# Performance work log

Measured on AMD Instinct MI355X. Metric: run time of the kernel, lower is better.

## Reference

```python
import jax, jax.numpy as jnp
import numpy as np

B = 8
WS = 7; NH = 8; HD = 16; C = 128; HP = 56; SHIFT = 3; L = HP * HP
SCALE = HD ** -0.5


def _rel_pos_index():
    coords = np.stack(np.meshgrid(np.arange(WS), np.arange(WS), indexing='ij')).reshape(2, -1)
    rel = (coords[:, :, None] - coords[:, None, :]).transpose(1, 2, 0)
    rel[:, :, 0] += WS - 1
    rel[:, :, 1] += WS - 1
    rel[:, :, 0] *= 2 * WS - 1
    return rel.sum(-1)  # (49, 49) int


def _attn_mask():
    img = np.zeros((HP, HP))
    cnt = 0
    for h in (slice(0, -WS), slice(-WS, -SHIFT), slice(-SHIFT, None)):
        for w in (slice(0, -WS), slice(-WS, -SHIFT), slice(-SHIFT, None)):
            img[h, w] = cnt
            cnt += 1
    m = img.reshape(HP // WS, WS, HP // WS, WS).transpose(0, 2, 1, 3).reshape(-1, WS * WS)
    am = m[:, None, :] - m[:, :, None]
    return np.where(am != 0, -100.0, 0.0).astype(np.float32)  # (64, 49, 49)


REL_IDX = _rel_pos_index()
ATTN_MASK = jnp.asarray(_attn_mask())


def _ln(x, g, b):
    mu = x.mean(-1, keepdims=True)
    v = ((x - mu) ** 2).mean(-1, keepdims=True)
    return (x - mu) / jnp.sqrt(v + 1e-5) * g + b


def setup_inputs() -> dict:
    key = jax.random.key(0)
    ks = iter(jax.random.split(key, 40))
    n = lambda shape: jax.random.normal(next(ks), shape, dtype=jnp.float32) * 0.02
    z = lambda shape: jnp.zeros(shape, dtype=jnp.float32)
    o = lambda shape: jnp.ones(shape, dtype=jnp.float32)
    return dict(
        infrared=jax.random.normal(next(ks), (B, 1, 224, 224), dtype=jnp.float32),
        visible=jax.random.normal(next(ks), (B, 1, 224, 224), dtype=jnp.float32),
        patch_w=n((16, C)), patch_b=z((C,)),
        pn_g=o((C,)), pn_b=z((C,)),
        pos_embed=n((1, L, C)),
        norm1_g=o((2, C)), norm1_b=z((2, C)),
        qkv_w=n((2, C, 3 * C)), qkv_b=z((2, 3 * C)),
        proj_w=n((2, C, C)), proj_b=z((2, C)),
        norm2_g=o((2, C)), norm2_b=z((2, C)),
        fc1_w=n((2, C, 4 * C)), fc1_b=z((2, 4 * C)),
        fc2_w=n((2, 4 * C, C)), fc2_b=z((2, C)),
        rpb=n((2, (2 * WS - 1) ** 2, NH)),
        normf_g=o((C,)), normf_b=z((C,)),
        head1_w=n((C, 256)), head1_b=z((256,)),
        head2_w=n((256, 1)), head2_b=z((1,)),
    )


def reference(infrared, visible, patch_w, patch_b, pn_g, pn_b, pos_embed,
              norm1_g, norm1_b, qkv_w, qkv_b, proj_w, proj_b,
              norm2_g, norm2_b, fc1_w, fc1_b, fc2_w, fc2_b, rpb,
              normf_g, normf_b, head1_w, head1_b, head2_w, head2_b):
    Bv = visible.shape[0]
    # 4x4 stride-4 conv on 1-channel input == patchify + matmul
    x = visible.reshape(Bv, HP, 4, HP, 4).transpose(0, 1, 3, 2, 4).reshape(Bv, L, 16)
    x = _ln(x @ patch_w + patch_b, pn_g, pn_b) + pos_embed  # (B, 3136, 128)

    def win_attn(xw, i, mask):
        Bn, N = xw.shape[0], WS * WS
        qkv = (xw @ qkv_w[i] + qkv_b[i]).reshape(Bn, N, 3, NH, HD).transpose(2, 0, 3, 1, 4)
        q, k, v = qkv[0], qkv[1], qkv[2]
        attn = jnp.einsum('bhnd,bhmd->bhnm', q * SCALE, k)  # (Bn, H, 49, 49)
        bias = rpb[i][REL_IDX.reshape(-1)].reshape(N, N, NH).transpose(2, 0, 1)
        attn = attn + bias[None]
        if mask is not None:
            attn = attn.reshape(Bv, -1, NH, N, N) + mask[None, :, None]
            attn = attn.reshape(Bn, NH, N, N)
        attn = jax.nn.softmax(attn, axis=-1)
        out = jnp.einsum('bhnm,bhmd->bhnd', attn, v).transpose(0, 2, 1, 3).reshape(Bn, N, C)
        return out @ proj_w[i] + proj_b[i]

    def block(x, i, shift):
        shortcut = x
        h = _ln(x, norm1_g[i], norm1_b[i]).reshape(Bv, HP, HP, C)
        if shift:
            h = jnp.roll(h, (-SHIFT, -SHIFT), (1, 2))
        w = h.reshape(Bv, 8, WS, 8, WS, C).transpose(0, 1, 3, 2, 4, 5).reshape(-1, WS * WS, C)
        w = win_attn(w, i, ATTN_MASK if shift else None)
        h = w.reshape(Bv, 8, 8, WS, WS, C).transpose(0, 1, 3, 2, 4, 5).reshape(Bv, HP, HP, C)
        if shift:
            h = jnp.roll(h, (SHIFT, SHIFT), (1, 2))
        x = shortcut + h.reshape(Bv, L, C)  # drop_path is identity at inference
        m = _ln(x, norm2_g[i], norm2_b[i])
        m = jax.nn.gelu(m @ fc1_w[i] + fc1_b[i]) @ fc2_w[i] + fc2_b[i]
        return x + m

    x = block(x, 0, False)
    x = block(x, 1, True)
    x = jax.nn.relu(_ln(x, normf_g, normf_b))          # (B, 3136, 128)
    x = x.reshape(Bv, C, HP, HP)                       # raw view, as in torch code
    x = jnp.repeat(jnp.repeat(x, 4, axis=2), 4, axis=3)  # nearest 56 -> 224
    x = x.reshape(Bv, 224 * 224, C)                    # raw view
    x = jax.nn.relu(x @ head1_w + head1_b) @ head2_w + head2_b
    return x.reshape(Bv, 1, 224, 224)
```

## Files before the change

### kernel.cpp

```cpp
#include <hip/hip_runtime.h>
#include <math.h>

#define DEV __device__ __forceinline__

constexpr int B_   = 8;
constexpr int NTOK = 25088;
constexpr int WGc  = 512;
constexpr int N2c  = 49;
constexpr int HDc  = 16;
constexpr int NHc  = 8;
constexpr float SCALEq = 0.25f;

typedef _Float16 f16x8 __attribute__((ext_vector_type(8)));
typedef float    f32x4 __attribute__((ext_vector_type(4)));

DEV float wave_sum(float v) {
#pragma unroll
  for (int m = 32; m >= 1; m >>= 1) v += __shfl_xor(v, m);
  return v;
}

DEV float gelu_f(float x) {
  float y = 0.7978845608028654f * (x + 0.044715f * x * x * x);
  return x / (1.f + __expf(-2.f * y));
}

DEV int win_map(int row, int shift) {
  int wg = row / 49, n = row - wg * 49;
  int b = wg >> 6, win = wg & 63;
  int sh = ((win >> 3) * 7) + n / 7;
  int sw = ((win & 7) * 7) + (n % 7);
  sh += shift; if (sh >= 56) sh -= 56;
  sw += shift; if (sw >= 56) sw -= 56;
  return b * 3136 + sh * 56 + sw;
}

DEV void split8(const float* __restrict__ x, ushort* hp, ushort* lp) {
  f16x8 h, l;
#pragma unroll
  for (int j = 0; j < 8; ++j) {
    float v = x[j];
    _Float16 hh = (_Float16)v;
    h[j] = hh;
    l[j] = (_Float16)(v - (float)hh);
  }
  *(f16x8*)hp = h;
  *(f16x8*)lp = l;
}

__global__ __launch_bounds__(128)
void patch_k(const float* __restrict__ vis, const float* __restrict__ pw,
             const float* __restrict__ pb, const float* __restrict__ g,
             const float* __restrict__ bb, const float* __restrict__ pos,
             float* __restrict__ X) {
  int row = blockIdx.x;
  int c = threadIdx.x;
  int b = row / 3136, l = row - b * 3136;
  int hp = l / 56, wp = l - hp * 56;
  __shared__ float p[16];
  __shared__ float red[2];
  if (c < 16) {
    int r = c >> 2, cc = c & 3;
    p[c] = vis[(long)b * 50176 + (hp * 4 + r) * 224 + wp * 4 + cc];
  }
  __syncthreads();
  float t = pb[c];
#pragma unroll
  for (int k = 0; k < 16; ++k) t = fmaf(p[k], pw[k * 128 + c], t);
  float s = wave_sum(t);
  if ((c & 63) == 0) red[c >> 6] = s;
  __syncthreads();
  float mu = (red[0] + red[1]) * (1.f / 128.f);
  __syncthreads();
  float d = t - mu;
  float s2 = wave_sum(d * d);
  if ((c & 63) == 0) red[c >> 6] = s2;
  __syncthreads();
  float var = (red[0] + red[1]) * (1.f / 128.f);
  float o = d * rsqrtf(var + 1e-5f) * g[c] + bb[c] + pos[(long)l * 128 + c];
  X[(long)row * 128 + c] = o;
}

__global__ __launch_bounds__(256)
void ln_k(const float* __restrict__ Xi, float* __restrict__ Out,
          const float* __restrict__ g, const float* __restrict__ b, int do_relu) {
  int row = blockIdx.x * 4 + (threadIdx.x >> 6);
  int lane = threadIdx.x & 63;
  long base = (long)row * 128 + lane * 2;
  float2 v = *(const float2*)&Xi[base];
  float mu = wave_sum(v.x + v.y) * (1.f / 128.f);
  float dx = v.x - mu, dy = v.y - mu;
  float var = wave_sum(dx * dx + dy * dy) * (1.f / 128.f);
  float r = rsqrtf(var + 1e-5f);
  float2 gg = *(const float2*)&g[lane * 2];
  float2 bb = *(const float2*)&b[lane * 2];
  float ox = dx * r * gg.x + bb.x;
  float oy = dy * r * gg.y + bb.y;
  if (do_relu) { ox = fmaxf(ox, 0.f); oy = fmaxf(oy, 0.f); }
  *(float2*)&Out[base] = make_float2(ox, oy);
}

template<int OUT_MODE, int ACT, int GATHER_A>
__global__ __launch_bounds__(256)
void mgemm_k(const float* __restrict__ A, const float* __restrict__ W,
             const float* __restrict__ bias, float* __restrict__ Out,
             int N, int K, int lda, int shift) {
  __shared__ __align__(16) ushort Ah[2048], Al[2048];
  __shared__ __align__(16) ushort Bh[4096], Bl[4096];
  int tid = threadIdx.x;
  int m0 = blockIdx.x * 64, n0 = blockIdx.y * 128;
  int lane = tid & 63, wid = tid >> 6;
  int wm = wid >> 1, wn = wid & 1;

  f32x4 acc[2][4];
#pragma unroll
  for (int mi = 0; mi < 2; ++mi)
#pragma unroll
    for (int ni = 0; ni < 4; ++ni) acc[mi][ni] = (f32x4){0.f, 0.f, 0.f, 0.f};

  int sr = tid >> 2;
  int sk8 = tid & 3;
  long asrc = GATHER_A ? (long)win_map(m0 + sr, shift) * lda
                       : (long)(m0 + sr) * lda;
  int achunk = ((sr >> 4) * 64 + sk8 * 16 + (sr & 15)) * 8;

  int bn0_ = tid & 127, bk80 = tid >> 7;
  int bn1_ = bn0_, bk81 = bk80 + 2;
  int bchunk0 = ((bn0_ >> 4) * 64 + bk80 * 16 + (bn0_ & 15)) * 8;
  int bchunk1 = ((bn1_ >> 4) * 64 + bk81 * 16 + (bn1_ & 15)) * 8;

  float areg[8], breg0[8], breg1[8];
  auto loadA = [&](int k0) {
    float4 t0 = *(const float4*)&A[asrc + k0 + sk8 * 8];
    float4 t1 = *(const float4*)&A[asrc + k0 + sk8 * 8 + 4];
    areg[0] = t0.x; areg[1] = t0.y; areg[2] = t0.z; areg[3] = t0.w;
    areg[4] = t1.x; areg[5] = t1.y; areg[6] = t1.z; areg[7] = t1.w;
  };
  auto loadB = [&](int k0) {
#pragma unroll
    for (int j = 0; j < 8; ++j)
      breg0[j] = W[(long)(k0 + bk80 * 8 + j) * N + n0 + bn0_];
#pragma unroll
    for (int j = 0; j < 8; ++j)
      breg1[j] = W[(long)(k0 + bk81 * 8 + j) * N + n0 + bn1_];
  };

  loadA(0); loadB(0);
  for (int k0 = 0; k0 < K; k0 += 32) {
    __syncthreads();
    split8(areg, &Ah[achunk], &Al[achunk]);
    split8(breg0, &Bh[bchunk0], &Bl[bchunk0]);
    split8(breg1, &Bh[bchunk1], &Bl[bchunk1]);
    __syncthreads();
    if (k0 + 32 < K) { loadA(k0 + 32); loadB(k0 + 32); }

    f16x8 ah[2], al[2], bh[4], bl[4];
#pragma unroll
    for (int mi = 0; mi < 2; ++mi) {
      int c = ((wm * 2 + mi) * 64 + lane) * 8;
      ah[mi] = *(const f16x8*)&Ah[c];
      al[mi] = *(const f16x8*)&Al[c];
    }
#pragma unroll
    for (int ni = 0; ni < 4; ++ni) {
      int c = ((wn * 4 + ni) * 64 + lane) * 8;
      bh[ni] = *(const f16x8*)&Bh[c];
      bl[ni] = *(const f16x8*)&Bl[c];
    }
#pragma unroll
    for (int mi = 0; mi < 2; ++mi)
#pragma unroll
      for (int ni = 0; ni < 4; ++ni) {
        acc[mi][ni] = __builtin_amdgcn_mfma_f32_16x16x32_f16(ah[mi], bh[ni], acc[mi][ni], 0, 0, 0);
        acc[mi][ni] = __builtin_amdgcn_mfma_f32_16x16x32_f16(ah[mi], bl[ni], acc[mi][ni], 0, 0, 0);
        acc[mi][ni] = __builtin_amdgcn_mfma_f32_16x16x32_f16(al[mi], bh[ni], acc[mi][ni], 0, 0, 0);
      }
  }

  int r4 = (lane >> 4) * 4, cb = lane & 15;
#pragma unroll
  for (int mi = 0; mi < 2; ++mi) {
#pragma unroll
    for (int rr = 0; rr < 4; ++rr) {
      int row = m0 + wm * 32 + mi * 16 + r4 + rr;
      int dst = (OUT_MODE == 2) ? win_map(row, shift) : row;
#pragma unroll
      for (int ni = 0; ni < 4; ++ni) {
        int col = n0 + wn * 64 + ni * 16 + cb;
        float val = acc[mi][ni][rr] + bias[col];
        if (ACT == 1) val = gelu_f(val);
        if (OUT_MODE == 0) {
          Out[(long)row * N + col] = val;
        } else if (OUT_MODE == 1) {
          int t = col >> 7, cc = col & 127, h = cc >> 4, d = cc & 15;
          if (t == 0) val *= SCALEq;
          int wg = row / 49, n = row - wg * 49;
          Out[((((long)t * WGc + wg) * NHc + h) * N2c + n) * HDc + d] = val;
        } else {
          Out[(long)dst * 128 + col] += val;
        }
      }
    }
  }
}

__global__ __launch_bounds__(256)
void attn_k(const float* __restrict__ QKV, float* __restrict__ AO,
            const float* __restrict__ rpb, int shift) {
  int wg = blockIdx.x >> 3;
  int h  = blockIdx.x & 7;
  int tid = threadIdx.x;
  __shared__ float Qs[49][17], Ks[49][17], Vs[49][17];
  __shared__ float S[49][50];
  const float* Qp = QKV + (((long)0 * WGc + wg) * NHc + h) * N2c * HDc;
  const float* Kp = QKV + (((long)1 * WGc + wg) * NHc + h) * N2c * HDc;
  const float* Vp = QKV + (((long)2 * WGc + wg) * NHc + h) * N2c * HDc;
  for (int idx = tid; idx < 49 * 16; idx += 256) {
    int n = idx >> 4, d = idx & 15;
    Qs[n][d] = Qp[idx]; Ks[n][d] = Kp[idx]; Vs[n][d] = Vp[idx];
  }
  __syncthreads();
  int win = wg & 63, wy = win >> 3, wx = win & 7;
  for (int idx = tid; idx < 49 * 49; idx += 256) {
    int i = idx / 49, j = idx - i * 49;
    float s = 0.f;
#pragma unroll
    for (int d = 0; d < 16; ++d) s = fmaf(Qs[i][d], Ks[j][d], s);
    int pyi = i / 7, pxi = i - pyi * 7, pyj = j / 7, pxj = j - pyj * 7;
    int rel = (pyi - pyj + 6) * 13 + (pxi - pxj + 6);
    s += rpb[rel * 8 + h];
    if (shift) {
      int shi = wy * 7 + pyi, swi = wx * 7 + pxi;
      int shj = wy * 7 + pyj, swj = wx * 7 + pxj;
      int ri = (shi < 49 ? 0 : (shi < 53 ? 1 : 2)) * 3 + (swi < 49 ? 0 : (swi < 53 ? 1 : 2));
      int rj = (shj < 49 ? 0 : (shj < 53 ? 1 : 2)) * 3 + (swj < 49 ? 0 : (swj < 53 ? 1 : 2));
      if (ri != rj) s -= 100.f;
    }
    S[i][j] = s;
  }
  __syncthreads();
  int lane = tid & 63, wv = tid >> 6;
  for (int i = wv; i < 49; i += 4) {
    float v = lane < 49 ? S[i][lane] : -1e30f;
    float m = v;
#pragma unroll
    for (int d = 32; d >= 1; d >>= 1) m = fmaxf(m, __shfl_xor(m, d));
    float e = lane < 49 ? __expf(v - m) : 0.f;
    float s = e;
#pragma unroll
    for (int d = 32; d >= 1; d >>= 1) s += __shfl_xor(s, d);
    if (lane < 49) S[i][lane] = e / s;
  }
  __syncthreads();
  for (int idx = tid; idx < 49 * 16; idx += 256) {
    int i = idx >> 4, d = idx & 15;
    float o = 0.f;
    for (int j = 0; j < 49; ++j) o = fmaf(S[i][j], Vs[j][d], o);
    AO[((long)wg * 49 + i) * 128 + h * 16 + d] = o;
  }
}

__global__ __launch_bounds__(256)
void w1sum_k(const float* __restrict__ W1, float* __restrict__ W1s) {
  int a = blockIdx.x, c = threadIdx.x;
  float s = W1[(4 * a + 0) * 256 + c] + W1[(4 * a + 1) * 256 + c] +
            W1[(4 * a + 2) * 256 + c] + W1[(4 * a + 3) * 256 + c];
  W1s[a * 256 + c] = s;
}

__global__ __launch_bounds__(512)
void head_k(const float* __restrict__ Y, const float* __restrict__ W1s,
            const float* __restrict__ b1, const float* __restrict__ W2,
            const float* __restrict__ b2, float* __restrict__ Out) {
  __shared__ float As[32][128];
  __shared__ float Ws[32][256];
  int tid = threadIdx.x;
  int m0 = blockIdx.x * 128;

  {
    int arow = tid >> 2;
    int rg = m0 + arow;
    int b = rg / 50176;
    int r = rg - b * 50176;
    int ch = r / 392;
    int s = r - ch * 392;
    long ybase = (long)b * 401408 + (long)ch * 3136;
    int a0 = (tid & 3) * 8;
    int tb = s * 128 + a0 * 4;
#pragma unroll
    for (int e = 0; e < 8; ++e) {
      int t = tb + e * 4;
      int H = t / 224, Wp = t - H * 224;
      As[a0 + e][arow] = Y[ybase + (H >> 2) * 56 + (Wp >> 2)];
    }
  }
  for (int i = tid; i < 2048; i += 512) {
    int id4 = i * 4;
    *(float4*)&Ws[id4 >> 8][id4 & 255] = *(const float4*)&W1s[id4];
  }
  __syncthreads();

  int tx = tid & 31, ty = tid >> 5;
  float acc[8][8] = {};
#pragma unroll 4
  for (int k = 0; k < 32; ++k) {
    float4 a0 = *(const float4*)&As[k][ty * 8];
    float4 a1 = *(const float4*)&As[k][ty * 8 + 4];
    float a8[8] = {a0.x, a0.y, a0.z, a0.w, a1.x, a1.y, a1.z, a1.w};
    float w8[8];
#pragma unroll
    for (int cc = 0; cc < 8; ++cc) w8[cc] = Ws[k][tx + 32 * cc];
#pragma unroll
    for (int rr = 0; rr < 8; ++rr)
#pragma unroll
      for (int cc = 0; cc < 8; ++cc)
        acc[rr][cc] = fmaf(a8[rr], w8[cc], acc[rr][cc]);
  }

  float b2v = b2[0];
#pragma unroll
  for (int rr = 0; rr < 8; ++rr) {
    float p = 0.f;
#pragma unroll
    for (int cc = 0; cc < 8; ++cc) {
      int col = tx + 32 * cc;
      float hval = fmaxf(acc[rr][cc] + b1[col], 0.f);
      p = fmaf(hval, W2[col], p);
    }
#pragma unroll
    for (int d = 16; d >= 1; d >>= 1) p += __shfl_xor(p, d);
    if (tx == 0) Out[(long)m0 + ty * 8 + rr] = p + b2v;
  }
}

extern "C" void kernel_launch(void* const* d_in, const int* in_sizes, int n_in,
                              void* d_out, int out_size, void* d_ws, size_t ws_size,
                              hipStream_t stream) {
  const float* visible = (const float*)d_in[1];
  const float* patch_w = (const float*)d_in[2];
  const float* patch_b = (const float*)d_in[3];
  const float* pn_g    = (const float*)d_in[4];
  const float* pn_b    = (const float*)d_in[5];
  const float* pos     = (const float*)d_in[6];
  const float* norm1_g = (const float*)d_in[7];
  const float* norm1_b = (const float*)d_in[8];
  const float* qkv_w   = (const float*)d_in[9];
  const float* qkv_b   = (const float*)d_in[10];
  const float* proj_w  = (const float*)d_in[11];
  const float* proj_b  = (const float*)d_in[12];
  const float* norm2_g = (const float*)d_in[13];
  const float* norm2_b = (const float*)d_in[14];
  const float* fc1_w   = (const float*)d_in[15];
  const float* fc1_b   = (const float*)d_in[16];
  const float* fc2_w   = (const float*)d_in[17];
  const float* fc2_b   = (const float*)d_in[18];
  const float* rpb     = (const float*)d_in[19];
  const float* normf_g = (const float*)d_in[20];
  const float* normf_b = (const float*)d_in[21];
  const float* h1w     = (const float*)d_in[22];
  const float* h1b     = (const float*)d_in[23];
  const float* h2w     = (const float*)d_in[24];
  const float* h2b     = (const float*)d_in[25];
  float* out = (float*)d_out;

  float* X   = (float*)d_ws;
  float* XN  = X  + (long)NTOK * 128;
  float* BIG = XN + (long)NTOK * 128;
  float* QKV = BIG;
  float* AO  = BIG + (long)NTOK * 384;
  float* Hb  = BIG;
  float* Y   = XN;
  float* W1s = BIG;

  patch_k<<<NTOK, 128, 0, stream>>>(visible, patch_w, patch_b, pn_g, pn_b, pos, X);

  for (int layer = 0; layer < 2; ++layer) {
    int shift = layer ? 3 : 0;
    ln_k<<<NTOK / 4, 256, 0, stream>>>(X, XN, norm1_g + layer * 128, norm1_b + layer * 128, 0);
    mgemm_k<1, 0, 1><<<dim3(392, 3), 256, 0, stream>>>(
        XN, qkv_w + (long)layer * 128 * 384, qkv_b + layer * 384, QKV, 384, 128, 128, shift);
    attn_k<<<WGc * 8, 256, 0, stream>>>(QKV, AO, rpb + (long)layer * 169 * 8, shift);
    mgemm_k<2, 0, 0><<<dim3(392, 1), 256, 0, stream>>>(
        AO, proj_w + (long)layer * 128 * 128, proj_b + layer * 128, X, 128, 128, 128, shift);
    ln_k<<<NTOK / 4, 256, 0, stream>>>(X, XN, norm2_g + layer * 128, norm2_b + layer * 128, 0);
    mgemm_k<0, 1, 0><<<dim3(392, 4), 256, 0, stream>>>(
        XN, fc1_w + (long)layer * 128 * 512, fc1_b + layer * 512, Hb, 512, 128, 128, 0);
    mgemm_k<3, 0, 0><<<dim3(392, 1), 256, 0, stream>>>(
        Hb, fc2_w + (long)layer * 512 * 128, fc2_b + layer * 128, X, 128, 512, 512, 0);
  }

  ln_k<<<NTOK / 4, 256, 0, stream>>>(X, Y, normf_g, normf_b, 1);
  w1sum_k<<<32, 256, 0, stream>>>(h1w, W1s);
  head_k<<<3136, 512, 0, stream>>>(Y, W1s, h1b, h2w, h2b, out);
}
```

Measured before the change: 537.4 us.

## Move head GEMM to fp16 MFMA with hi/lo split for fp32 accuracy

```diff
diff --git a/kernel.cpp b/kernel.cpp
--- a/kernel.cpp
+++ b/kernel.cpp
@@ -261,75 +261,83 @@
 }
 
 __global__ __launch_bounds__(256)
-void w1sum_k(const float* __restrict__ W1, float* __restrict__ W1s) {
+void w1split_k(const float* __restrict__ W1, ushort* __restrict__ Bh_g,
+               ushort* __restrict__ Bl_g) {
   int a = blockIdx.x, c = threadIdx.x;
   float s = W1[(4 * a + 0) * 256 + c] + W1[(4 * a + 1) * 256 + c] +
             W1[(4 * a + 2) * 256 + c] + W1[(4 * a + 3) * 256 + c];
-  W1s[a * 256 + c] = s;
-}
-
-__global__ __launch_bounds__(512)
-void head_k(const float* __restrict__ Y, const float* __restrict__ W1s,
-            const float* __restrict__ b1, const float* __restrict__ W2,
-            const float* __restrict__ b2, float* __restrict__ Out) {
-  __shared__ float As[32][128];
-  __shared__ float Ws[32][256];
+  _Float16 h = (_Float16)s;
+  _Float16 l = (_Float16)(s - (float)h);
+  int idx = ((c >> 4) * 64 + (a >> 3) * 16 + (c & 15)) * 8 + (a & 7);
+  Bh_g[idx] = *(const ushort*)&h;
+  Bl_g[idx] = *(const ushort*)&l;
+}
+
+__global__ __launch_bounds__(256)
+void head_mfma_k(const float* __restrict__ Y, const ushort* __restrict__ Bh_g,
+                 const ushort* __restrict__ Bl_g, const float* __restrict__ b1,
+                 const float* __restrict__ W2, const float* __restrict__ b2,
+                 float* __restrict__ Out) {
+  __shared__ __align__(16) ushort Ah[2048], Al[2048];
+  __shared__ __align__(16) ushort Bh[8192], Bl[8192];
   int tid = threadIdx.x;
-  int m0 = blockIdx.x * 128;
+  int m0 = blockIdx.x * 64;
+  int lane = tid & 63, w = tid >> 6;
 
   {
-    int arow = tid >> 2;
-    int rg = m0 + arow;
+    int sr = tid >> 2, sk8 = tid & 3;
+    int rg = m0 + sr;
     int b = rg / 50176;
     int r = rg - b * 50176;
     int ch = r / 392;
     int s = r - ch * 392;
     long ybase = (long)b * 401408 + (long)ch * 3136;
-    int a0 = (tid & 3) * 8;
-    int tb = s * 128 + a0 * 4;
-#pragma unroll
-    for (int e = 0; e < 8; ++e) {
-      int t = tb + e * 4;
+    float av[8];
+#pragma unroll
+    for (int j = 0; j < 8; ++j) {
+      int t = s * 128 + (sk8 * 8 + j) * 4;
       int H = t / 224, Wp = t - H * 224;
-      As[a0 + e][arow] = Y[ybase + (H >> 2) * 56 + (Wp >> 2)];
-    }
-  }
-  for (int i = tid; i < 2048; i += 512) {
-    int id4 = i * 4;
-    *(float4*)&Ws[id4 >> 8][id4 & 255] = *(const float4*)&W1s[id4];
-  }
-  __syncthreads();
-
-  int tx = tid & 31, ty = tid >> 5;
-  float acc[8][8] = {};
-#pragma unroll 4
-  for (int k = 0; k < 32; ++k) {
-    float4 a0 = *(const float4*)&As[k][ty * 8];
-    float4 a1 = *(const float4*)&As[k][ty * 8 + 4];
-    float a8[8] = {a0.x, a0.y, a0.z, a0.w, a1.x, a1.y, a1.z, a1.w};
-    float w8[8];
-#pragma unroll
-    for (int cc = 0; cc < 8; ++cc) w8[cc] = Ws[k][tx + 32 * cc];
-#pragma unroll
-    for (int rr = 0; rr < 8; ++rr)
-#pragma unroll
-      for (int cc = 0; cc < 8; ++cc)
-        acc[rr][cc] = fmaf(a8[rr], w8[cc], acc[rr][cc]);
-  }
-
+      av[j] = Y[ybase + (H >> 2) * 56 + (Wp >> 2)];
+    }
+    int chunk = ((sr >> 4) * 64 + sk8 * 16 + (sr & 15)) * 8;
+    split8(av, &Ah[chunk], &Al[chunk]);
+  }
+  for (int i = tid; i < 1024; i += 256) {
+    *(f16x8*)&Bh[i * 8] = *(const f16x8*)&Bh_g[i * 8];
+    *(f16x8*)&Bl[i * 8] = *(const f16x8*)&Bl_g[i * 8];
+  }
+  float b1v[16], w2v[16];
+#pragma unroll
+  for (int ni = 0; ni < 16; ++ni) {
+    b1v[ni] = b1[ni * 16 + (lane & 15)];
+    w2v[ni] = W2[ni * 16 + (lane & 15)];
+  }
+  __syncthreads();
+
+  f16x8 ah = *(const f16x8*)&Ah[(w * 64 + lane) * 8];
+  f16x8 al = *(const f16x8*)&Al[(w * 64 + lane) * 8];
+  float p[4] = {0.f, 0.f, 0.f, 0.f};
+#pragma unroll
+  for (int ni = 0; ni < 16; ++ni) {
+    f16x8 bh = *(const f16x8*)&Bh[(ni * 64 + lane) * 8];
+    f16x8 bl = *(const f16x8*)&Bl[(ni * 64 + lane) * 8];
+    f32x4 acc = (f32x4){0.f, 0.f, 0.f, 0.f};
+    acc = __builtin_amdgcn_mfma_f32_16x16x32_f16(ah, bh, acc, 0, 0, 0);
+    acc = __builtin_amdgcn_mfma_f32_16x16x32_f16(ah, bl, acc, 0, 0, 0);
+    acc = __builtin_amdgcn_mfma_f32_16x16x32_f16(al, bh, acc, 0, 0, 0);
+#pragma unroll
+    for (int reg = 0; reg < 4; ++reg) {
+      float hval = fmaxf(acc[reg] + b1v[ni], 0.f);
+      p[reg] = fmaf(hval, w2v[ni], p[reg]);
+    }
+  }
   float b2v = b2[0];
 #pragma unroll
-  for (int rr = 0; rr < 8; ++rr) {
-    float p = 0.f;
-#pragma unroll
-    for (int cc = 0; cc < 8; ++cc) {
-      int col = tx + 32 * cc;
-      float hval = fmaxf(acc[rr][cc] + b1[col], 0.f);
-      p = fmaf(hval, W2[col], p);
-    }
-#pragma unroll
-    for (int d = 16; d >= 1; d >>= 1) p += __shfl_xor(p, d);
-    if (tx == 0) Out[(long)m0 + ty * 8 + rr] = p + b2v;
+  for (int reg = 0; reg < 4; ++reg) {
+#pragma unroll
+    for (int d = 1; d < 16; d <<= 1) p[reg] += __shfl_xor(p[reg], d);
+    if ((lane & 15) == 0)
+      Out[m0 + w * 16 + (lane >> 4) * 4 + reg] = p[reg] + b2v;
   }
 }
 
@@ -370,7 +378,8 @@
   float* AO  = BIG + (long)NTOK * 384;
   float* Hb  = BIG;
   float* Y   = XN;
-  float* W1s = BIG;
+  ushort* BHG = (ushort*)BIG;
+  ushort* BLG = BHG + 8192;
 
   patch_k<<<NTOK, 128, 0, stream>>>(visible, patch_w, patch_b, pn_g, pn_b, pos, X);
 
@@ -390,6 +399,6 @@
   }
 
   ln_k<<<NTOK / 4, 256, 0, stream>>>(X, Y, normf_g, normf_b, 1);
-  w1sum_k<<<32, 256, 0, stream>>>(h1w, W1s);
-  head_k<<<3136, 512, 0, stream>>>(Y, W1s, h1b, h2w, h2b, out);
-}
+  w1split_k<<<32, 256, 0, stream>>>(h1w, BHG, BLG);
+  head_mfma_k<<<6272, 256, 0, stream>>>(Y, BHG, BLG, h1b, h2w, h2b, out);
+}
```

Result: faster. 485.4 us (-9.7%).
